# Kernel optimization log

Measured on AMD Instinct MI355X. Metric: run time of the kernel, lower is better.

Reference implementation:

```python
import jax, jax.numpy as jnp
import numpy as np

NUM_HEADS = 16

def setup_inputs() -> dict:
    key = jax.random.key(0)
    ks = jax.random.split(key, 6)
    b, t, d = 2, 2048, 1024
    s = 0.02
    return {
        "x": jax.random.normal(ks[0], (b, t, d), jnp.float32),
        "Wq": jax.random.normal(ks[1], (d, d), jnp.float32) * s,
        "Wk": jax.random.normal(ks[2], (d, d), jnp.float32) * s,
        "Wv": jax.random.normal(ks[3], (d, d), jnp.float32) * s,
        "Wo": jax.random.normal(ks[4], (d, d), jnp.float32) * s,
        "bo": jnp.zeros((d,), jnp.float32),
    }

def reference(x, Wq, Wk, Wv, Wo, bo):
    b, t, d = x.shape
    h = NUM_HEADS
    hd = d // h  # head_dim = d_out / num_heads
    # torch nn.Linear: y = x @ W.T (qkv_bias=False)
    def split_heads(y):
        return y.reshape(b, t, h, hd).transpose(0, 2, 1, 3)  # [b,h,t,hd]
    q = split_heads(x @ Wq.T)
    k = split_heads(x @ Wk.T)
    v = split_heads(x @ Wv.T)
    scale = 1.0 / jnp.sqrt(jnp.asarray(hd, x.dtype))
    # NOTE: original forward computes but never applies the causal mask or dropout
    scores = jnp.einsum('bhqd,bhkd->bhqk', q, k) * scale
    attn = jax.nn.softmax(scores, axis=-1)
    ctx = jnp.einsum('bhqk,bhkd->bhqd', attn, v)
    ctx = ctx.transpose(0, 2, 1, 3).reshape(b, t, d)
    return ctx @ Wo.T + bo
```

## Files before the change

### kernel.cpp

```cpp
#include <hip/hip_runtime.h>
#include <hip/hip_bf16.h>
#include <math.h>
#include <stdint.h>
#include <string.h>

#define TSEQ 2048
#define DMODEL 1024
#define NH 16
#define HD 64
#define BROWS 4096
#define BH 32

typedef __attribute__((ext_vector_type(8))) short short8;
typedef __attribute__((ext_vector_type(4))) float floatx4;

#define MFMA16 __builtin_amdgcn_mfma_f32_16x16x32_bf16
#define SWZ8(r, q) ((((q) ^ ((r) & 7)) * 8))

#define QSCALE 0.18033688011112042f

__device__ __forceinline__ unsigned short bf16_rne(float f) {
    uint32_t u = __float_as_uint(f);
    u += 0x7FFFu + ((u >> 16) & 1u);
    return (unsigned short)(u >> 16);
}

__device__ __forceinline__ uint32_t pack_bf16x2(float a, float b) {
    __hip_bfloat162 h = __float22bfloat162_rn(float2{a, b});
    uint32_t r;
    memcpy(&r, &h, 4);
    return r;
}

__device__ __forceinline__ void split_bf16(float f, short& hi, short& lo) {
    uint32_t u = __float_as_uint(f);
    hi = (short)(u >> 16);
    float hif = __uint_as_float(u & 0xFFFF0000u);
    lo = (short)bf16_rne(f - hif);
}

__device__ __forceinline__ void async16(const void* g, void* l) {
    __builtin_amdgcn_global_load_lds(
        (__attribute__((address_space(1))) const uint32_t*)g,
        (__attribute__((address_space(3))) uint32_t*)l, 16, 0, 0);
}

struct PackArgs {
    const float4* x;
    ushort4* xb;
    const float4* w[3];
    ushort4* wb[3];
    const float4* wo;
    ushort4* woh;
    ushort4* wol;
};
__global__ __launch_bounds__(256) void pack_all(PackArgs a) {
    const int y = blockIdx.y;
    const int base = blockIdx.x * 256 + threadIdx.x;
    if (y == 0) {
#pragma unroll
        for (int it = 0; it < 4; ++it) {
            int i = base + it * 262144;
            float4 f = a.x[i];
            a.xb[i] = make_ushort4(bf16_rne(f.x), bf16_rne(f.y),
                                   bf16_rne(f.z), bf16_rne(f.w));
        }
    } else if (y <= 3) {
        int w = y - 1;
        float4 f = a.w[w][base];
        a.wb[w][base] = make_ushort4(bf16_rne(f.x), bf16_rne(f.y),
                                     bf16_rne(f.z), bf16_rne(f.w));
    } else {
        float4 f = a.wo[base];
        short h0, l0, h1, l1, h2, l2, h3, l3;
        split_bf16(f.x, h0, l0); split_bf16(f.y, h1, l1);
        split_bf16(f.z, h2, l2); split_bf16(f.w, h3, l3);
        a.woh[base] = make_ushort4(h0, h1, h2, h3);
        a.wol[base] = make_ushort4(l0, l1, l2, l3);
    }
}

#define QSTAGE(DB, K0)                                                          \
    {                                                                           \
        _Pragma("unroll")                                                       \
        for (int j = 0; j < 8; ++j) {                                           \
            int idx = wave * 8 + j;                                             \
            int sub = idx & 15;                                                 \
            const short* s = (idx < 16) ? Asrc : Bsrc;                          \
            short* d = (idx < 16) ? sA[DB] : sB[DB];                            \
            async16(s + (size_t)(sub * 8 + srow) * K + (K0) + soff, d + sub * 512); \
        }                                                                       \
    }

__global__ __launch_bounds__(256) void gemm_qkv(
    const short* __restrict__ Xb,
    const short* __restrict__ Bq, const short* __restrict__ Bk,
    const short* __restrict__ Bv,
    short* __restrict__ Qo, short* __restrict__ Ko, short* __restrict__ Vo) {
    __shared__ short sA[2][128 * 64];
    __shared__ short sB[2][128 * 64];
    const int K = DMODEL;

    const int tid = threadIdx.x;
    const int lane = tid & 63, wave = tid >> 6;
    const int quad = lane >> 4, col = lane & 15;

    const int lin = blockIdx.y * 24 + blockIdx.x;
    const int xcd = lin & 7, j8 = lin >> 3;
    const int bxp = 3 * xcd + (j8 % 3);
    const int byp = j8 / 3;
    const int m0 = byp * 128, n0 = bxp * 128;
    const int which = n0 >> 10;
    const int nn0 = n0 & 1023;
    const int wm = wave >> 1, wn = wave & 1;

    const short* B = (which == 0) ? Bq : (which == 1) ? Bk : Bv;
    const short* Asrc = Xb + (size_t)m0 * K;
    const short* Bsrc = B + (size_t)nn0 * K;

    const int srow = lane >> 3;
    const int soff = (((lane & 7) ^ srow) * 8);

    floatx4 acc[4][4] = {};

    QSTAGE(0, 0);
    for (int t = 0; t < 16; ++t) {
        const int db = t & 1;
        if (t < 15) {
            QSTAGE(db ^ 1, (t + 1) * 64);
            asm volatile("s_waitcnt vmcnt(8)" ::: "memory");
        } else {
            asm volatile("s_waitcnt vmcnt(0)" ::: "memory");
        }
        __builtin_amdgcn_s_barrier();

#pragma unroll
        for (int s2 = 0; s2 < 2; ++s2) {
            short8 a_b[4], b_b[4];
#pragma unroll
            for (int mi = 0; mi < 4; ++mi) {
                int r = wm * 64 + mi * 16 + col;
                a_b[mi] = *(const short8*)&sA[db][r * 64 + SWZ8(r, s2 * 4 + quad)];
            }
#pragma unroll
            for (int ni = 0; ni < 4; ++ni) {
                int r = wn * 64 + ni * 16 + col;
                b_b[ni] = *(const short8*)&sB[db][r * 64 + SWZ8(r, s2 * 4 + quad)];
            }
            __builtin_amdgcn_s_setprio(1);
            if (which == 2) {
#pragma unroll
                for (int mi = 0; mi < 4; ++mi)
#pragma unroll
                    for (int ni = 0; ni < 4; ++ni)
                        acc[mi][ni] = MFMA16(a_b[mi], b_b[ni], acc[mi][ni], 0, 0, 0);
            } else {
#pragma unroll
                for (int mi = 0; mi < 4; ++mi)
#pragma unroll
                    for (int ni = 0; ni < 4; ++ni)
                        acc[mi][ni] = MFMA16(b_b[ni], a_b[mi], acc[mi][ni], 0, 0, 0);
            }
            __builtin_amdgcn_s_setprio(0);
        }
        __builtin_amdgcn_s_barrier();
    }

    const int mb = m0 + wm * 64;
    const int nlb = nn0 + wn * 64;
    if (which == 2) {
#pragma unroll
        for (int ni = 0; ni < 4; ++ni) {
            int n = nlb + ni * 16 + col;
            int h = n >> 6, hd = n & 63;
#pragma unroll
            for (int mi = 0; mi < 4; ++mi) {
                int m4 = mb + mi * 16 + quad * 4;
                int b = m4 >> 11, t0 = m4 & 2047;
                int sw = (t0 & 32) | ((t0 & 12) << 1) | ((t0 & 16) >> 2);
                int tsw = (t0 & ~63) | ((((sw >> 3) ^ (hd & 7)) << 3) | (sw & 7));
                size_t row = ((size_t)(b * NH + h) * HD + hd) * TSEQ;
                *(ushort4*)&Vo[row + tsw] =
                    make_ushort4(bf16_rne(acc[mi][ni][0]), bf16_rne(acc[mi][ni][1]),
                                 bf16_rne(acc[mi][ni][2]), bf16_rne(acc[mi][ni][3]));
            }
        }
    } else {
        short* O = (which == 0) ? Qo : Ko;
        const float sc = (which == 0) ? QSCALE : 1.0f;
#pragma unroll
        for (int mi = 0; mi < 4; ++mi) {
            int m = mb + mi * 16 + col;
            int b = m >> 11, t = m & 2047;
#pragma unroll
            for (int ni = 0; ni < 4; ++ni) {
                int n = nlb + ni * 16 + quad * 4;
                int h = n >> 6, hd = n & 63;
                int hds = (which == 1) ? ((((hd >> 3) ^ (t & 7)) << 3) | (hd & 7)) : hd;
                size_t idx = ((size_t)(b * NH + h) * TSEQ + t) * HD + hds;
                *(ushort4*)&O[idx] =
                    make_ushort4(bf16_rne(acc[mi][ni][0] * sc), bf16_rne(acc[mi][ni][1] * sc),
                                 bf16_rne(acc[mi][ni][2] * sc), bf16_rne(acc[mi][ni][3] * sc));
            }
        }
    }
}

#define ATTN_COMPUTE(DB)                                                        \
    {                                                                           \
        _Pragma("unroll")                                                       \
        for (int u = 0; u < 2; ++u) {                                           \
            floatx4 s[4] = {};                                                  \
            __builtin_amdgcn_s_setprio(1);                                      \
            _Pragma("unroll")                                                   \
            for (int k4 = 0; k4 < 4; ++k4) {                                    \
                short8 kf0 = *(const short8*)(kb0 + (DB) * 8192 + u * 4096 + k4 * 1024); \
                short8 kf1 = *(const short8*)(kb1 + (DB) * 8192 + u * 4096 + k4 * 1024); \
                s[k4] = MFMA16(kf0, qf[0], s[k4], 0, 0, 0);                     \
                s[k4] = MFMA16(kf1, qf[1], s[k4], 0, 0, 0);                     \
            }                                                                   \
            __builtin_amdgcn_s_setprio(0);                                      \
            float p[4][4];                                                      \
            _Pragma("unroll")                                                   \
            for (int k4 = 0; k4 < 4; ++k4)                                      \
                _Pragma("unroll")                                               \
                for (int r4 = 0; r4 < 4; ++r4)                                  \
                    p[k4][r4] = __builtin_amdgcn_exp2f(s[k4][r4]);              \
            _Pragma("unroll")                                                   \
            for (int c = 0; c < 2; ++c) {                                       \
                union { short8 v; uint32_t w[4]; } pf;                          \
                pf.w[0] = pack_bf16x2(p[2 * c][0], p[2 * c][1]);                \
                pf.w[1] = pack_bf16x2(p[2 * c][2], p[2 * c][3]);                \
                pf.w[2] = pack_bf16x2(p[2 * c + 1][0], p[2 * c + 1][1]);        \
                pf.w[3] = pack_bf16x2(p[2 * c + 1][2], p[2 * c + 1][3]);        \
                const short* vbc = c ? vb1 : vb0;                               \
                __builtin_amdgcn_s_setprio(1);                                  \
                lacc = MFMA16(ones.v, pf.v, lacc, 0, 0, 0);                     \
                _Pragma("unroll")                                               \
                for (int ni = 0; ni < 4; ++ni) {                                \
                    short8 vf = *(const short8*)(vbc + (DB) * 8192 + u * 4096 + ni * 1024); \
                    O[ni] = MFMA16(vf, pf.v, O[ni], 0, 0, 0);                   \
                }                                                               \
                __builtin_amdgcn_s_setprio(0);                                  \
            }                                                                   \
        }                                                                       \
    }

#define ASTAGE(LB)                                                              \
    {                                                                           \
        async16(g0, (LB) + 0 * 512);                                            \
        async16(g1, (LB) + 1 * 512);                                            \
        async16(g2, (LB) + 2 * 512);                                            \
        async16(g3, (LB) + 3 * 512);                                            \
        g0 += ktstep; g1 += ktstep; g2 += ktstep; g3 += ktstep;                 \
    }

__global__ __launch_bounds__(512, 4) void attn_bf16(
    const short* __restrict__ Qb, const short* __restrict__ Kb,
    const short* __restrict__ Vb, short* __restrict__ Cb) {
    __shared__ short sK[2][2][64 * 64];
    __shared__ short sV[2][2][64 * 64];

    const int tid = threadIdx.x;
    const int lane = tid & 63, wave = tid >> 6;
    const int quad = lane >> 4, col = lane & 15;

    const int lin = blockIdx.y * 16 + blockIdx.x;
    const int xcd = lin & 7, j8 = lin >> 3;
    const int qt = j8 & 15;
    const int bh = 4 * xcd + (j8 >> 4);
    const size_t bhoff = (size_t)bh * TSEQ * HD;

    const size_t qrow = (size_t)(qt * 128 + wave * 16 + col) * HD;
    short8 qf[2];
#pragma unroll
    for (int c = 0; c < 2; ++c)
        qf[c] = *(const short8*)&Qb[bhoff + qrow + c * 32 + quad * 8];

    const int srow = lane >> 3;
    const int schunk = (lane & 7) * 8;

    const int isV = wave >> 2;
    const int tl = (wave >> 1) & 1;
    const int sb = (wave & 1) * 4;

    const short *g0, *g1, *g2, *g3;
    size_t ktstep;
    if (!isV) {
        g0 = Kb + bhoff + (size_t)(tl * 64 + (sb + 0) * 8 + srow) * HD + schunk;
        g1 = Kb + bhoff + (size_t)(tl * 64 + (sb + 1) * 8 + srow) * HD + schunk;
        g2 = Kb + bhoff + (size_t)(tl * 64 + (sb + 2) * 8 + srow) * HD + schunk;
        g3 = Kb + bhoff + (size_t)(tl * 64 + (sb + 3) * 8 + srow) * HD + schunk;
        ktstep = (size_t)128 * HD;
    } else {
        g0 = Vb + bhoff + (size_t)((sb + 0) * 8 + srow) * TSEQ + tl * 64 + schunk;
        g1 = Vb + bhoff + (size_t)((sb + 1) * 8 + srow) * TSEQ + tl * 64 + schunk;
        g2 = Vb + bhoff + (size_t)((sb + 2) * 8 + srow) * TSEQ + tl * 64 + schunk;
        g3 = Vb + bhoff + (size_t)((sb + 3) * 8 + srow) * TSEQ + tl * 64 + schunk;
        ktstep = 128;
    }
    short* lb0_ = isV ? &sV[0][tl][sb * 512] : &sK[0][tl][sb * 512];
    short* lb1_ = isV ? &sV[1][tl][sb * 512] : &sK[1][tl][sb * 512];

    const int ch0 = ((quad ^ (col & 7)) << 3);
    const int ch1 = (((4 + quad) ^ (col & 7)) << 3);
    const short* kb0 = &sK[0][0][col * 64 + ch0];
    const short* kb1 = &sK[0][0][col * 64 + ch1];
    const short* vb0 = &sV[0][0][col * 64 + ch0];
    const short* vb1 = &sV[0][0][col * 64 + ch1];

    union { short8 v; short s[8]; } ones;
#pragma unroll
    for (int j = 0; j < 8; ++j) ones.s[j] = (short)0x3F80;

    floatx4 lacc = {};
    floatx4 O[4] = {};

    ASTAGE(lb0_);

    for (int kt2 = 0; kt2 < 8; ++kt2) {
        ASTAGE(lb1_);
        asm volatile("s_waitcnt vmcnt(4)" ::: "memory");
        __builtin_amdgcn_s_barrier();
        ATTN_COMPUTE(0);
        __builtin_amdgcn_s_barrier();

        if (kt2 < 7) {
            ASTAGE(lb0_);
            asm volatile("s_waitcnt vmcnt(4)" ::: "memory");
        } else {
            asm volatile("s_waitcnt vmcnt(0)" ::: "memory");
        }
        __builtin_amdgcn_s_barrier();
        ATTN_COMPUTE(1);
        __builtin_amdgcn_s_barrier();
    }

    const float inv = 1.0f / lacc[0];

    const int b = bh >> 4, h = bh & 15;
    const int trow = qt * 128 + wave * 16 + col;
    const size_t obase = (size_t)(b * TSEQ + trow) * DMODEL + h * 64;
#pragma unroll
    for (int ni = 0; ni < 4; ++ni) {
        uint2 pk;
        pk.x = pack_bf16x2(O[ni][0] * inv, O[ni][1] * inv);
        pk.y = pack_bf16x2(O[ni][2] * inv, O[ni][3] * inv);
        *(uint2*)&Cb[obase + ni * 16 + quad * 4] = pk;
    }
}

#define OSTAGE(DB, K0)                                                          \
    {                                                                           \
        _Pragma("unroll")                                                       \
        for (int j = 0; j < 8; ++j) {                                           \
            int idx = wave * 8 + j;                                             \
            int buf = (idx < 16) ? 0 : (idx < 24) ? 1 : 2;                      \
            int sub = (buf == 0) ? idx : (buf == 1) ? idx - 16 : idx - 24;      \
            const short* s = (buf == 0) ? Asrc : (buf == 1) ? Bhsrc : Blsrc;    \
            short* d = (buf == 0) ? sA[DB] : (buf == 1) ? sBh[DB] : sBl[DB];    \
            async16(s + (size_t)(sub * 8 + srow) * K + (K0) + soff, d + sub * 512); \
        }                                                                       \
    }

__global__ __launch_bounds__(256) void gemm_out(
    const short* __restrict__ Ab,
    const short* __restrict__ Bh, const short* __restrict__ Bl,
    const float* __restrict__ bias, float* __restrict__ Of) {
    __shared__ short sA[2][128 * 64];
    __shared__ short sBh[2][64 * 64];
    __shared__ short sBl[2][64 * 64];
    const int K = DMODEL, N = DMODEL;

    const int tid = threadIdx.x;
    const int lane = tid & 63, wave = tid >> 6;
    const int quad = lane >> 4, col = lane & 15;

    const int lin = blockIdx.y * 16 + blockIdx.x;
    const int xcd = lin & 7, j8 = lin >> 3;
    const int bxp = 2 * xcd + (j8 & 1);
    const int byp = j8 >> 1;
    const int m0 = byp * 128, n0 = bxp * 64;
    const int wm = wave >> 1, wn = wave & 1;

    const short* Asrc = Ab + (size_t)m0 * K;
    const short* Bhsrc = Bh + (size_t)n0 * K;
    const short* Blsrc = Bl + (size_t)n0 * K;
    const int srow = lane >> 3;
    const int soff = (((lane & 7) ^ srow) * 8);

    floatx4 acc[4][2] = {};

    OSTAGE(0, 0);
    for (int t = 0; t < 16; ++t) {
        const int db = t & 1;
        if (t < 15) {
            OSTAGE(db ^ 1, (t + 1) * 64);
            asm volatile("s_waitcnt vmcnt(8)" ::: "memory");
        } else {
            asm volatile("s_waitcnt vmcnt(0)" ::: "memory");
        }
        __builtin_amdgcn_s_barrier();

#pragma unroll
        for (int s2 = 0; s2 < 2; ++s2) {
            short8 a_b[4], b_h[2], b_l[2];
#pragma unroll
            for (int mi = 0; mi < 4; ++mi) {
                int r = wm * 64 + mi * 16 + col;
                a_b[mi] = *(const short8*)&sA[db][r * 64 + SWZ8(r, s2 * 4 + quad)];
            }
#pragma unroll
            for (int ni = 0; ni < 2; ++ni) {
                int r = wn * 32 + ni * 16 + col;
                b_h[ni] = *(const short8*)&sBh[db][r * 64 + SWZ8(r, s2 * 4 + quad)];
                b_l[ni] = *(const short8*)&sBl[db][r * 64 + SWZ8(r, s2 * 4 + quad)];
            }
            __builtin_amdgcn_s_setprio(1);
#pragma unroll
            for (int mi = 0; mi < 4; ++mi)
#pragma unroll
                for (int ni = 0; ni < 2; ++ni) {
                    acc[mi][ni] = MFMA16(b_h[ni], a_b[mi], acc[mi][ni], 0, 0, 0);
                    acc[mi][ni] = MFMA16(b_l[ni], a_b[mi], acc[mi][ni], 0, 0, 0);
                }
            __builtin_amdgcn_s_setprio(0);
        }
        __builtin_amdgcn_s_barrier();
    }

    const int mb = m0 + wm * 64, nb = n0 + wn * 32;
#pragma unroll
    for (int mi = 0; mi < 4; ++mi) {
        int m = mb + mi * 16 + col;
#pragma unroll
        for (int ni = 0; ni < 2; ++ni) {
            int n = nb + ni * 16 + quad * 4;
            float4 bv = *(const float4*)&bias[n];
            float4 o = make_float4(acc[mi][ni][0] + bv.x, acc[mi][ni][1] + bv.y,
                                   acc[mi][ni][2] + bv.z, acc[mi][ni][3] + bv.w);
            *(float4*)&Of[(size_t)m * N + n] = o;
        }
    }
}

extern "C" void kernel_launch(void* const* d_in, const int* in_sizes, int n_in,
                              void* d_out, int out_size, void* d_ws, size_t ws_size,
                              hipStream_t stream) {
    const float* x  = (const float*)d_in[0];
    const float* Wq = (const float*)d_in[1];
    const float* Wk = (const float*)d_in[2];
    const float* Wv = (const float*)d_in[3];
    const float* Wo = (const float*)d_in[4];
    const float* bo = (const float*)d_in[5];
    float* out = (float*)d_out;

    const size_t NX = (size_t)BROWS * DMODEL;
    const size_t NW = (size_t)DMODEL * DMODEL;
    short* p = (short*)d_ws;
    short *xb = p;
    short *wqb = xb + NX;
    short *wkb = wqb + NW;
    short *wvb = wkb + NW;
    short *woh = wvb + NW; short *wol = woh + NW;
    short *qb = wol + NW;
    short *kb = qb + NX;
    short *vb = kb + NX;
    short *cb = vb + NX;

    PackArgs pa;
    pa.x = (const float4*)x; pa.xb = (ushort4*)xb;
    pa.w[0] = (const float4*)Wq; pa.wb[0] = (ushort4*)wqb;
    pa.w[1] = (const float4*)Wk; pa.wb[1] = (ushort4*)wkb;
    pa.w[2] = (const float4*)Wv; pa.wb[2] = (ushort4*)wvb;
    pa.wo = (const float4*)Wo; pa.woh = (ushort4*)woh; pa.wol = (ushort4*)wol;
    pack_all<<<dim3(1024, 5), dim3(256), 0, stream>>>(pa);

    gemm_qkv<<<dim3(3 * DMODEL / 128, BROWS / 128), dim3(256), 0, stream>>>(
        xb, wqb, wkb, wvb, qb, kb, vb);

    attn_bf16<<<dim3(TSEQ / 128, BH), dim3(512), 0, stream>>>(qb, kb, vb, cb);

    gemm_out<<<dim3(DMODEL / 64, BROWS / 128), dim3(256), 0, stream>>>(cb, woh, wol, bo, out);
}
```

Measured before the change: 183.0 us.

## Use 8-wave QKV GEMM blocks, software-pipeline attention exp with PV, drop XCD remap

The QKV projection GEMM now runs 512 threads per block. Each of its 8 waves computes a 32x64 sub-tile instead of 64x64 and issues half as many async loads per stage. The aim is to raise occupancy and cut per-wave register pressure, at the cost of more LDS fragment reloads per MFMA. The attention inner loop is reordered so the second QK^T tile and its exp/pack are interleaved with the first P·V MFMAs, overlapping transcendental work with matrix ops. The XCD-aware block remapping in attention is removed in favour of plain blockIdx indexing, which may lose L2 locality for K/V.

Result: no change. 180.4 us (-1.4%).

```diff
diff --git a/kernel.cpp b/kernel.cpp
--- a/kernel.cpp
+++ b/kernel.cpp
@@ -83,8 +83,8 @@
 #define QSTAGE(DB, K0)                                                          \
     {                                                                           \
         _Pragma("unroll")                                                       \
-        for (int j = 0; j < 8; ++j) {                                           \
-            int idx = wave * 8 + j;                                             \
+        for (int j = 0; j < 4; ++j) {                                           \
+            int idx = wave * 4 + j;                                             \
             int sub = idx & 15;                                                 \
             const short* s = (idx < 16) ? Asrc : Bsrc;                          \
             short* d = (idx < 16) ? sA[DB] : sB[DB];                            \
@@ -92,7 +92,7 @@
         }                                                                       \
     }
 
-__global__ __launch_bounds__(256) void gemm_qkv(
+__global__ __launch_bounds__(512, 4) void gemm_qkv(
     const short* __restrict__ Xb,
     const short* __restrict__ Bq, const short* __restrict__ Bk,
     const short* __restrict__ Bv,
@@ -121,14 +121,14 @@
     const int srow = lane >> 3;
     const int soff = (((lane & 7) ^ srow) * 8);
 
-    floatx4 acc[4][4] = {};
+    floatx4 acc[2][4] = {};
 
     QSTAGE(0, 0);
     for (int t = 0; t < 16; ++t) {
         const int db = t & 1;
         if (t < 15) {
             QSTAGE(db ^ 1, (t + 1) * 64);
-            asm volatile("s_waitcnt vmcnt(8)" ::: "memory");
+            asm volatile("s_waitcnt vmcnt(4)" ::: "memory");
         } else {
             asm volatile("s_waitcnt vmcnt(0)" ::: "memory");
         }
@@ -136,10 +136,10 @@
 
 #pragma unroll
         for (int s2 = 0; s2 < 2; ++s2) {
-            short8 a_b[4], b_b[4];
-#pragma unroll
-            for (int mi = 0; mi < 4; ++mi) {
-                int r = wm * 64 + mi * 16 + col;
+            short8 a_b[2], b_b[4];
+#pragma unroll
+            for (int mi = 0; mi < 2; ++mi) {
+                int r = wm * 32 + mi * 16 + col;
                 a_b[mi] = *(const short8*)&sA[db][r * 64 + SWZ8(r, s2 * 4 + quad)];
             }
 #pragma unroll
@@ -150,13 +150,13 @@
             __builtin_amdgcn_s_setprio(1);
             if (which == 2) {
 #pragma unroll
-                for (int mi = 0; mi < 4; ++mi)
+                for (int mi = 0; mi < 2; ++mi)
 #pragma unroll
                     for (int ni = 0; ni < 4; ++ni)
                         acc[mi][ni] = MFMA16(a_b[mi], b_b[ni], acc[mi][ni], 0, 0, 0);
             } else {
 #pragma unroll
-                for (int mi = 0; mi < 4; ++mi)
+                for (int mi = 0; mi < 2; ++mi)
 #pragma unroll
                     for (int ni = 0; ni < 4; ++ni)
                         acc[mi][ni] = MFMA16(b_b[ni], a_b[mi], acc[mi][ni], 0, 0, 0);
@@ -166,7 +166,7 @@
         __builtin_amdgcn_s_barrier();
     }
 
-    const int mb = m0 + wm * 64;
+    const int mb = m0 + wm * 32;
     const int nlb = nn0 + wn * 64;
     if (which == 2) {
 #pragma unroll
@@ -174,7 +174,7 @@
             int n = nlb + ni * 16 + col;
             int h = n >> 6, hd = n & 63;
 #pragma unroll
-            for (int mi = 0; mi < 4; ++mi) {
+            for (int mi = 0; mi < 2; ++mi) {
                 int m4 = mb + mi * 16 + quad * 4;
                 int b = m4 >> 11, t0 = m4 & 2047;
                 int sw = (t0 & 32) | ((t0 & 12) << 1) | ((t0 & 16) >> 2);
@@ -189,7 +189,7 @@
         short* O = (which == 0) ? Qo : Ko;
         const float sc = (which == 0) ? QSCALE : 1.0f;
 #pragma unroll
-        for (int mi = 0; mi < 4; ++mi) {
+        for (int mi = 0; mi < 2; ++mi) {
             int m = mb + mi * 16 + col;
             int b = m >> 11, t = m & 2047;
 #pragma unroll
@@ -206,44 +206,67 @@
     }
 }
 
+#define QK_U(DB, U, S)                                                          \
+    {                                                                           \
+        __builtin_amdgcn_s_setprio(1);                                          \
+        _Pragma("unroll")                                                       \
+        for (int k4 = 0; k4 < 4; ++k4) {                                        \
+            short8 kf0 = *(const short8*)(kb0 + (DB) * 8192 + (U) * 4096 + k4 * 1024); \
+            short8 kf1 = *(const short8*)(kb1 + (DB) * 8192 + (U) * 4096 + k4 * 1024); \
+            S[k4] = MFMA16(kf0, qf[0], S[k4], 0, 0, 0);                         \
+            S[k4] = MFMA16(kf1, qf[1], S[k4], 0, 0, 0);                         \
+        }                                                                       \
+        __builtin_amdgcn_s_setprio(0);                                          \
+    }
+
+#define EXPPACK_C(S, C, PFW)                                                    \
+    {                                                                           \
+        float p0 = __builtin_amdgcn_exp2f(S[2 * (C)][0]);                       \
+        float p1 = __builtin_amdgcn_exp2f(S[2 * (C)][1]);                       \
+        float p2 = __builtin_amdgcn_exp2f(S[2 * (C)][2]);                       \
+        float p3 = __builtin_amdgcn_exp2f(S[2 * (C)][3]);                       \
+        float p4 = __builtin_amdgcn_exp2f(S[2 * (C) + 1][0]);                   \
+        float p5 = __builtin_amdgcn_exp2f(S[2 * (C) + 1][1]);                   \
+        float p6 = __builtin_amdgcn_exp2f(S[2 * (C) + 1][2]);                   \
+        float p7 = __builtin_amdgcn_exp2f(S[2 * (C) + 1][3]);                   \
+        PFW.w[0] = pack_bf16x2(p0, p1);                                         \
+        PFW.w[1] = pack_bf16x2(p2, p3);                                         \
+        PFW.w[2] = pack_bf16x2(p4, p5);                                         \
+        PFW.w[3] = pack_bf16x2(p6, p7);                                         \
+    }
+
+#define PV_C(DB, U, C, PFW)                                                     \
+    {                                                                           \
+        const short* vbc = (C) ? vb1 : vb0;                                     \
+        __builtin_amdgcn_s_setprio(1);                                          \
+        lacc = MFMA16(ones.v, PFW.v, lacc, 0, 0, 0);                            \
+        _Pragma("unroll")                                                       \
+        for (int ni = 0; ni < 4; ++ni) {                                        \
+            short8 vf = *(const short8*)(vbc + (DB) * 8192 + (U) * 4096 + ni * 1024); \
+            O[ni] = MFMA16(vf, PFW.v, O[ni], 0, 0, 0);                          \
+        }                                                                       \
+        __builtin_amdgcn_s_setprio(0);                                          \
+    }
+
+typedef union { short8 v; uint32_t w[4]; } pfu;
+
 #define ATTN_COMPUTE(DB)                                                        \
     {                                                                           \
-        _Pragma("unroll")                                                       \
-        for (int u = 0; u < 2; ++u) {                                           \
-            floatx4 s[4] = {};                                                  \
-            __builtin_amdgcn_s_setprio(1);                                      \
-            _Pragma("unroll")                                                   \
-            for (int k4 = 0; k4 < 4; ++k4) {                                    \
-                short8 kf0 = *(const short8*)(kb0 + (DB) * 8192 + u * 4096 + k4 * 1024); \
-                short8 kf1 = *(const short8*)(kb1 + (DB) * 8192 + u * 4096 + k4 * 1024); \
-                s[k4] = MFMA16(kf0, qf[0], s[k4], 0, 0, 0);                     \
-                s[k4] = MFMA16(kf1, qf[1], s[k4], 0, 0, 0);                     \
-            }                                                                   \
-            __builtin_amdgcn_s_setprio(0);                                      \
-            float p[4][4];                                                      \
-            _Pragma("unroll")                                                   \
-            for (int k4 = 0; k4 < 4; ++k4)                                      \
-                _Pragma("unroll")                                               \
-                for (int r4 = 0; r4 < 4; ++r4)                                  \
-                    p[k4][r4] = __builtin_amdgcn_exp2f(s[k4][r4]);              \
-            _Pragma("unroll")                                                   \
-            for (int c = 0; c < 2; ++c) {                                       \
-                union { short8 v; uint32_t w[4]; } pf;                          \
-                pf.w[0] = pack_bf16x2(p[2 * c][0], p[2 * c][1]);                \
-                pf.w[1] = pack_bf16x2(p[2 * c][2], p[2 * c][3]);                \
-                pf.w[2] = pack_bf16x2(p[2 * c + 1][0], p[2 * c + 1][1]);        \
-                pf.w[3] = pack_bf16x2(p[2 * c + 1][2], p[2 * c + 1][3]);        \
-                const short* vbc = c ? vb1 : vb0;                               \
-                __builtin_amdgcn_s_setprio(1);                                  \
-                lacc = MFMA16(ones.v, pf.v, lacc, 0, 0, 0);                     \
-                _Pragma("unroll")                                               \
-                for (int ni = 0; ni < 4; ++ni) {                                \
-                    short8 vf = *(const short8*)(vbc + (DB) * 8192 + u * 4096 + ni * 1024); \
-                    O[ni] = MFMA16(vf, pf.v, O[ni], 0, 0, 0);                   \
-                }                                                               \
-                __builtin_amdgcn_s_setprio(0);                                  \
-            }                                                                   \
-        }                                                                       \
+        floatx4 sa[4] = {};                                                     \
+        QK_U(DB, 0, sa);                                                        \
+        pfu pfA0, pfA1;                                                         \
+        EXPPACK_C(sa, 0, pfA0);                                                 \
+        EXPPACK_C(sa, 1, pfA1);                                                 \
+        floatx4 sb[4] = {};                                                     \
+        QK_U(DB, 1, sb);                                                        \
+              \
+        pfu pfB0, pfB1;                                                         \
+        PV_C(DB, 0, 0, pfA0);                                                   \
+        EXPPACK_C(sb, 0, pfB0);                                                 \
+        PV_C(DB, 0, 1, pfA1);                                                   \
+        EXPPACK_C(sb, 1, pfB1);                                                 \
+        PV_C(DB, 1, 0, pfB0);                                                   \
+        PV_C(DB, 1, 1, pfB1);                                                   \
     }
 
 #define ASTAGE(LB)                                                              \
@@ -264,11 +287,7 @@
     const int tid = threadIdx.x;
     const int lane = tid & 63, wave = tid >> 6;
     const int quad = lane >> 4, col = lane & 15;
-
-    const int lin = blockIdx.y * 16 + blockIdx.x;
-    const int xcd = lin & 7, j8 = lin >> 3;
-    const int qt = j8 & 15;
-    const int bh = 4 * xcd + (j8 >> 4);
+    const int qt = blockIdx.x, bh = blockIdx.y;
     const size_t bhoff = (size_t)bh * TSEQ * HD;
 
     const size_t qrow = (size_t)(qt * 128 + wave * 16 + col) * HD;
@@ -476,7 +495,7 @@
     pa.wo = (const float4*)Wo; pa.woh = (ushort4*)woh; pa.wol = (ushort4*)wol;
     pack_all<<<dim3(1024, 5), dim3(256), 0, stream>>>(pa);
 
-    gemm_qkv<<<dim3(3 * DMODEL / 128, BROWS / 128), dim3(256), 0, stream>>>(
+    gemm_qkv<<<dim3(3 * DMODEL / 128, BROWS / 128), dim3(512), 0, stream>>>(
         xb, wqb, wkb, wvb, qb, kb, vb);
 
     attn_bf16<<<dim3(TSEQ / 128, BH), dim3(512), 0, stream>>>(qb, kb, vb, cb);
```
